# Performance work log

Measured on AMD Instinct MI355X. Metric: run time of the kernel, lower is better.

## Reference

```python
import jax, jax.numpy as jnp
import numpy as np

B, L, H, V = 2, 1024, 64, 32000
HID = 4 * H  # hidden_dim = num_harmonics * 4


def setup_inputs() -> dict:
    key = jax.random.key(0)
    ks = jax.random.split(key, 12)
    freqs = jax.random.normal(ks[0], (B, L, H), dtype=jnp.float32)
    amps = jax.random.uniform(ks[1], (B, L, H), dtype=jnp.float32)  # positive so log1p(sum) is finite
    phases = jax.random.normal(ks[2], (B, L, H), dtype=jnp.float32)
    wave_repr = jnp.concatenate([freqs, amps, phases], axis=-1)  # [B, L, 3H]
    s = 0.05
    return {
        "wave_repr": wave_repr,
        "vocab_frequencies": jax.random.normal(ks[3], (V, H), dtype=jnp.float32),
        "vocab_phases": jax.random.normal(ks[4], (V, H), dtype=jnp.float32) * 0.5,
        "W0": jax.random.normal(ks[5], (3 * H, HID), dtype=jnp.float32) * s,
        "b0": jnp.zeros((HID,), dtype=jnp.float32),
        "W1": jax.random.normal(ks[6], (HID, HID), dtype=jnp.float32) * s,
        "b1": jnp.zeros((HID,), dtype=jnp.float32),
        "W2": jax.random.normal(ks[7], (HID, HID), dtype=jnp.float32) * s,
        "b2": jnp.zeros((HID,), dtype=jnp.float32),
        "Wv": jax.random.normal(ks[8], (HID, V), dtype=jnp.float32) * s,
        "bv": jnp.zeros((V,), dtype=jnp.float32),
        "residual_weights": jnp.full((3,), 0.5, dtype=jnp.float32),
    }


def _gelu(x):
    return jax.nn.gelu(x, approximate=False)  # torch F.gelu default = exact erf


def reference(wave_repr, vocab_frequencies, vocab_phases, W0, b0, W1, b1, W2, b2, Wv, bv, residual_weights):
    h = vocab_frequencies.shape[1]
    freqs = wave_repr[..., :h]
    amps = wave_repr[..., h:2 * h]
    phases = wave_repr[..., 2 * h:]

    # synthesis MLP: layer 0 has no residual; layers 1..2 add weighted residual
    x = _gelu(wave_repr @ W0 + b0)
    for i, (W, b) in enumerate(((W1, b1), (W2, b2)), start=1):
        res = x
        x = _gelu(x @ W + b) + residual_weights[i] * res

    # freq_similarity = -cdist(freqs, vocab_frequencies): expanded as one GEMM
    f2 = jnp.sum(freqs * freqs, axis=-1, keepdims=True)           # [B,L,1]
    v2 = jnp.sum(vocab_frequencies * vocab_frequencies, axis=-1)  # [V]
    cross = jnp.einsum('blh,vh->blv', freqs, vocab_frequencies)   # [B,L,V]
    freq_similarity = -jnp.sqrt(jnp.maximum(f2 + v2 - 2.0 * cross, 0.0))

    # mean_h cos(phase - vocab_phase) via cos(a-b) = cos a cos b + sin a sin b (two GEMMs)
    phase_coherence = (
        jnp.einsum('blh,vh->blv', jnp.cos(phases), jnp.cos(vocab_phases))
        + jnp.einsum('blh,vh->blv', jnp.sin(phases), jnp.sin(vocab_phases))
    ) / h

    amp_energy = jnp.sum(amps, axis=-1, keepdims=True)  # [B,L,1]
    pattern_match = (freq_similarity + 0.5 * phase_coherence) * jnp.log1p(amp_energy)

    synthesis_proj = x @ Wv + bv  # [B,L,V]
    return pattern_match + 0.1 * synthesis_proj
```

## Files before the change

kernel.cpp:

```cpp
#include <hip/hip_runtime.h>
#include <hip/hip_bf16.h>

typedef unsigned short u16;
typedef __attribute__((ext_vector_type(8))) unsigned short u16x8;
typedef __attribute__((ext_vector_type(8))) short short8;
typedef __attribute__((ext_vector_type(4))) float f32x4;

#define VCOLS 32000
#define ASTRIDE 448
#define BSTRIDE 448

__device__ __forceinline__ u16 f2bf(float f) {
    union { float f; unsigned u; } x; x.f = f;
    unsigned r = x.u + 0x7FFF + ((x.u >> 16) & 1);
    return (u16)(r >> 16);
}

__device__ __forceinline__ float gelu_exact(float v) {
    return 0.5f * v * (1.0f + erff(v * 0.70710678118654752f));
}

__device__ __forceinline__ void gload_lds16(const void* g, void* l) {
    __builtin_amdgcn_global_load_lds(
        (const __attribute__((address_space(1))) unsigned int*)g,
        (__attribute__((address_space(3))) unsigned int*)l, 16, 0, 0);
}

#define RP_ROWS 8
__global__ __launch_bounds__(256) void row_prep(
    const float* __restrict__ wr,
    const float* __restrict__ W0, const float* __restrict__ b0,
    const float* __restrict__ W1, const float* __restrict__ b1,
    const float* __restrict__ W2, const float* __restrict__ b2,
    const float* __restrict__ rw,
    u16* __restrict__ Ag, float* __restrict__ rowstats)
{
    __shared__ float in_s[RP_ROWS * 192];
    __shared__ float x_s[RP_ROWS * 256];
    __shared__ float y_s[RP_ROWS * 256];
    __shared__ u16  row_s[RP_ROWS][448];
    __shared__ float la_s[RP_ROWS];

    const int t = threadIdx.x;
    const int r0 = blockIdx.x * RP_ROWS;

    for (int i = t; i < RP_ROWS * 192; i += 256)
        in_s[i] = wr[(size_t)r0 * 192 + i];
    __syncthreads();

    {
        int row = t >> 5, j = t & 31;
        float a0 = in_s[row*192 + j],      a1 = in_s[row*192 + 32 + j];
        float f2p = a0*a0 + a1*a1;
        float ampp = in_s[row*192 + 64 + j] + in_s[row*192 + 96 + j];
        #pragma unroll
        for (int m = 16; m >= 1; m >>= 1) {
            f2p  += __shfl_xor(f2p, m);
            ampp += __shfl_xor(ampp, m);
        }
        if (j == 0) {
            float la = log1pf(ampp);
            la_s[row] = la;
            rowstats[(size_t)(r0+row)*2]     = f2p;
            rowstats[(size_t)(r0+row)*2 + 1] = la;
        }
    }
    const float rw1 = rw[1], rw2 = rw[2];

    float acc[RP_ROWS], res[RP_ROWS];

    #pragma unroll
    for (int r = 0; r < RP_ROWS; ++r) acc[r] = 0.f;
    for (int k0 = 0; k0 < 192; k0 += 16) {
        float w[16];
        #pragma unroll
        for (int e = 0; e < 16; ++e) w[e] = W0[(k0+e)*256 + t];
        #pragma unroll
        for (int e = 0; e < 16; ++e) {
            #pragma unroll
            for (int r = 0; r < RP_ROWS; ++r) acc[r] += in_s[r*192 + k0 + e] * w[e];
        }
    }
    {
        float bb = b0[t];
        #pragma unroll
        for (int r = 0; r < RP_ROWS; ++r) {
            float v = gelu_exact(acc[r] + bb);
            res[r] = v; x_s[r*256 + t] = v;
        }
    }
    __syncthreads();

    #pragma unroll
    for (int r = 0; r < RP_ROWS; ++r) acc[r] = 0.f;
    for (int k0 = 0; k0 < 256; k0 += 16) {
        float w[16];
        #pragma unroll
        for (int e = 0; e < 16; ++e) w[e] = W1[(k0+e)*256 + t];
        #pragma unroll
        for (int e = 0; e < 16; ++e) {
            #pragma unroll
            for (int r = 0; r < RP_ROWS; ++r) acc[r] += x_s[r*256 + k0 + e] * w[e];
        }
    }
    {
        float bb = b1[t];
        #pragma unroll
        for (int r = 0; r < RP_ROWS; ++r) {
            float v = gelu_exact(acc[r] + bb) + rw1 * res[r];
            res[r] = v; y_s[r*256 + t] = v;
        }
    }
    __syncthreads();

    #pragma unroll
    for (int r = 0; r < RP_ROWS; ++r) acc[r] = 0.f;
    for (int k0 = 0; k0 < 256; k0 += 16) {
        float w[16];
        #pragma unroll
        for (int e = 0; e < 16; ++e) w[e] = W2[(k0+e)*256 + t];
        #pragma unroll
        for (int e = 0; e < 16; ++e) {
            #pragma unroll
            for (int r = 0; r < RP_ROWS; ++r) acc[r] += y_s[r*256 + k0 + e] * w[e];
        }
    }
    {
        float bb = b2[t];
        #pragma unroll
        for (int r = 0; r < RP_ROWS; ++r)
            res[r] = gelu_exact(acc[r] + bb) + rw2 * res[r];
    }

    #pragma unroll
    for (int r = 0; r < RP_ROWS; ++r)
        row_s[r][192 + t] = f2bf(0.1f * res[r]);
    if (t < 64) {
        #pragma unroll
        for (int r = 0; r < RP_ROWS; ++r)
            row_s[r][t] = f2bf(in_s[r*192 + t]);
    } else if (t < 128) {
        int h = t - 64;
        #pragma unroll
        for (int r = 0; r < RP_ROWS; ++r) {
            float s, c; __sincosf(in_s[r*192 + 128 + h], &s, &c);
            row_s[r][t] = f2bf(c * (0.5f/64.f) * la_s[r]);
        }
    } else if (t < 192) {
        int h = t - 128;
        #pragma unroll
        for (int r = 0; r < RP_ROWS; ++r) {
            float s, c; __sincosf(in_s[r*192 + 128 + h], &s, &c);
            row_s[r][t] = f2bf(s * (0.5f/64.f) * la_s[r]);
        }
    }
    __syncthreads();

    for (int idx = t; idx < RP_ROWS * 56; idx += 256) {
        int r = idx / 56, c = idx % 56;
        int kt = c >> 3, ac = c & 7;
        int m = r0 + r;
        u16x8 val = *(const u16x8*)&row_s[r][c*8];
        *(u16x8*)(Ag + (size_t)m*ASTRIDE + kt*64 + ((ac ^ (m & 7)) * 8)) = val;
    }
}

__global__ __launch_bounds__(256) void vocab_prep(
    const float* __restrict__ vf, const float* __restrict__ vp,
    const float* __restrict__ Wv,
    u16* __restrict__ Bg, float* __restrict__ v2)
{
    const int t = threadIdx.x;
    const int v0 = blockIdx.x * 64;

    {
        int v = v0 + (t >> 2);
        int q = t & 3;
        int s = v & 7;
        u16x8* baseB = (u16x8*)(Bg + (size_t)v * BSTRIDE);

        const float4* src = (const float4*)(vf + (size_t)v*64 + q*16);
        float ss = 0.f;
        u16 tf[16];
        #pragma unroll
        for (int i = 0; i < 4; ++i) {
            float4 x = src[i];
            ss += x.x*x.x + x.y*x.y + x.z*x.z + x.w*x.w;
            tf[i*4+0] = f2bf(x.x); tf[i*4+1] = f2bf(x.y);
            tf[i*4+2] = f2bf(x.z); tf[i*4+3] = f2bf(x.w);
        }
        u16x8 o0, o1;
        #pragma unroll
        for (int e = 0; e < 8; ++e) { o0[e] = tf[e]; o1[e] = tf[8+e]; }
        baseB[(2*q) ^ s]     = o0;
        baseB[(2*q+1) ^ s]   = o1;

        ss += __shfl_xor(ss, 1);
        ss += __shfl_xor(ss, 2);
        if (q == 0) v2[v] = ss;

        const float4* sp = (const float4*)(vp + (size_t)v*64 + q*16);
        u16 tc[16], ts_[16];
        #pragma unroll
        for (int i = 0; i < 4; ++i) {
            float4 x = sp[i];
            float sn, cs;
            __sincosf(x.x, &sn, &cs); tc[i*4+0] = f2bf(cs); ts_[i*4+0] = f2bf(sn);
            __sincosf(x.y, &sn, &cs); tc[i*4+1] = f2bf(cs); ts_[i*4+1] = f2bf(sn);
            __sincosf(x.z, &sn, &cs); tc[i*4+2] = f2bf(cs); ts_[i*4+2] = f2bf(sn);
            __sincosf(x.w, &sn, &cs); tc[i*4+3] = f2bf(cs); ts_[i*4+3] = f2bf(sn);
        }
        u16x8 c0, c1, s0, s1;
        #pragma unroll
        for (int e = 0; e < 8; ++e) { c0[e]=tc[e]; c1[e]=tc[8+e]; s0[e]=ts_[e]; s1[e]=ts_[8+e]; }
        baseB[8  + ((2*q) ^ s)]   = c0;
        baseB[8  + ((2*q+1) ^ s)] = c1;
        baseB[16 + ((2*q) ^ s)]   = s0;
        baseB[16 + ((2*q+1) ^ s)] = s1;
    }

    {
        int v  = v0 + (t & 63);
        int s  = v & 7;
        int kt = 3 + (t >> 6);
        int kb = (t >> 6) * 64;
        u16x8* baseB = (u16x8*)(Bg + (size_t)v * BSTRIDE);
        #pragma unroll
        for (int i = 0; i < 8; ++i) {
            u16 tmp[8];
            #pragma unroll
            for (int e = 0; e < 8; ++e)
                tmp[e] = f2bf(Wv[(size_t)(kb + i*8 + e) * VCOLS + v]);
            u16x8 o;
            #pragma unroll
            for (int e = 0; e < 8; ++e) o[e] = tmp[e];
            baseB[kt*8 + (i ^ s)] = o;
        }
    }
}

__global__ __launch_bounds__(256) void spectral_main(
    const u16* __restrict__ Ag, const u16* __restrict__ Bg,
    const float* __restrict__ rowstats, const float* __restrict__ v2,
    const float* __restrict__ bv, float* __restrict__ out)
{
    __shared__ u16 As[128 * 64];
    __shared__ u16 Bs[128 * 64];

    const int bid = blockIdx.x;
    const int l   = (bid & 7) * 500 + (bid >> 3);
    const int tm  = l / 250;
    const int tn  = l % 250;
    const int rowA0 = tm * 128;
    const int colB0 = tn * 128;

    const int tid  = threadIdx.x;
    const int wv   = tid >> 6, lane = tid & 63;
    const int wm   = (wv >> 1) * 64, wn = (wv & 1) * 64;
    const int cg   = lane >> 4, ln = lane & 15;

    f32x4 acc[4][4] = {};

    auto stage = [&](int kt) {
        const u16* ab = Ag + (size_t)(rowA0 + wv*32 + (lane >> 3)) * ASTRIDE + kt*64 + (lane & 7)*8;
        u16* al = As + wv*2048 + lane*8;
        #pragma unroll
        for (int c = 0; c < 4; ++c)
            gload_lds16(ab + (size_t)c*8*ASTRIDE, al + c*512);
        const u16* bb = Bg + (size_t)(colB0 + wv*32 + (lane >> 3)) * BSTRIDE + kt*64 + (lane & 7)*8;
        u16* bl = Bs + wv*2048 + lane*8;
        #pragma unroll
        for (int c = 0; c < 4; ++c)
            gload_lds16(bb + (size_t)c*8*BSTRIDE, bl + c*512);
    };

    auto compute = [&]() {
        #pragma unroll
        for (int kk = 0; kk < 2; ++kk) {
            short8 a[4], b[4];
            #pragma unroll
            for (int fr = 0; fr < 4; ++fr) {
                int r = wm + fr*16 + ln;
                a[fr] = *(const short8*)&As[r*64 + (((kk*4 + cg) ^ (ln & 7)) * 8)];
            }
            #pragma unroll
            for (int fc = 0; fc < 4; ++fc) {
                int r = wn + fc*16 + ln;
                b[fc] = *(const short8*)&Bs[r*64 + (((kk*4 + cg) ^ (ln & 7)) * 8)];
            }
            #pragma unroll
            for (int fr = 0; fr < 4; ++fr)
                #pragma unroll
                for (int fc = 0; fc < 4; ++fc)
                    acc[fr][fc] = __builtin_amdgcn_mfma_f32_16x16x32_bf16(
                        a[fr], b[fc], acc[fr][fc], 0, 0, 0);
        }
    };

    stage(0);
    __syncthreads();
    compute();

    {
        float f2m[4][4], lam[4][4], v2n[4], bvn[4];
        #pragma unroll
        for (int fr = 0; fr < 4; ++fr)
            #pragma unroll
            for (int j = 0; j < 4; ++j) {
                int m = rowA0 + wm + fr*16 + cg*4 + j;
                f2m[fr][j] = rowstats[(size_t)2*m];
                lam[fr][j] = rowstats[(size_t)2*m + 1];
            }
        #pragma unroll
        for (int fc = 0; fc < 4; ++fc) {
            int n = colB0 + wn + fc*16 + ln;
            v2n[fc] = v2[n];
            bvn[fc] = bv[n];
        }
        #pragma unroll
        for (int fr = 0; fr < 4; ++fr)
            #pragma unroll
            for (int fc = 0; fc < 4; ++fc)
                #pragma unroll
                for (int j = 0; j < 4; ++j) {
                    float cross = acc[fr][fc][j];
                    float arg = fmaxf(f2m[fr][j] + v2n[fc] - 2.0f*cross, 0.0f);
                    acc[fr][fc][j] = 0.1f*bvn[fc] - lam[fr][j]*sqrtf(arg);
                }
    }

    for (int kt = 1; kt < 7; ++kt) {
        __syncthreads();
        stage(kt);
        __syncthreads();
        compute();
    }

    #pragma unroll
    for (int fr = 0; fr < 4; ++fr)
        #pragma unroll
        for (int fc = 0; fc < 4; ++fc)
            #pragma unroll
            for (int j = 0; j < 4; ++j) {
                int m = rowA0 + wm + fr*16 + cg*4 + j;
                int n = colB0 + wn + fc*16 + ln;
                out[(size_t)m * VCOLS + n] = acc[fr][fc][j];
            }
}

extern "C" void kernel_launch(void* const* d_in, const int* in_sizes, int n_in,
                              void* d_out, int out_size, void* d_ws, size_t ws_size,
                              hipStream_t stream) {
    const float* wave_repr = (const float*)d_in[0];
    const float* vf  = (const float*)d_in[1];
    const float* vp  = (const float*)d_in[2];
    const float* W0  = (const float*)d_in[3];
    const float* b0  = (const float*)d_in[4];
    const float* W1  = (const float*)d_in[5];
    const float* b1  = (const float*)d_in[6];
    const float* W2  = (const float*)d_in[7];
    const float* b2  = (const float*)d_in[8];
    const float* Wv  = (const float*)d_in[9];
    const float* bv  = (const float*)d_in[10];
    const float* rw  = (const float*)d_in[11];
    float* out = (float*)d_out;

    u16*   Ag       = (u16*)d_ws;
    u16*   Bg       = (u16*)((char*)d_ws + 1835008);
    float* rowstats = (float*)((char*)d_ws + 30507008);
    float* v2       = (float*)((char*)d_ws + 30523392);

    hipLaunchKernelGGL(row_prep, dim3(2048 / RP_ROWS), dim3(256), 0, stream,
                       wave_repr, W0, b0, W1, b1, W2, b2, rw, Ag, rowstats);
    hipLaunchKernelGGL(vocab_prep, dim3(VCOLS / 64), dim3(256), 0, stream,
                       vf, vp, Wv, Bg, v2);
    hipLaunchKernelGGL(spectral_main, dim3(16 * 250), dim3(256), 0, stream,
                       Ag, Bg, rowstats, v2, bv, out);
}
```

Before: 470.3 us.

## Double-buffer LDS tiles in main GEMM and stage Wv transpose via shared memory

The main GEMM kernel now keeps two LDS buffers for its A and B tiles. It issues the global-to-LDS load for the next K tile before computing the current one, using explicit vmcnt waits and barriers, so memory latency overlaps with MFMA work. Launch bounds now request two blocks per CU. Separately, the vocab prep kernel reads Wv with coalesced float4 loads into a padded shared tile and transposes from there, replacing strided per-element global reads. The extra LDS per block could limit occupancy, and the hand-written waitcnt logic depends on how many loads are still outstanding.

Result: faster. 458.6 us (-2.5%).

```diff
diff --git a/kernel.cpp b/kernel.cpp
--- a/kernel.cpp
+++ b/kernel.cpp
@@ -170,6 +170,8 @@
     const float* __restrict__ Wv,
     u16* __restrict__ Bg, float* __restrict__ v2)
 {
+    __shared__ float wv_s[64][68];
+
     const int t = threadIdx.x;
     const int v0 = blockIdx.x * 64;
 
@@ -219,33 +221,38 @@
         baseB[16 + ((2*q+1) ^ s)] = s1;
     }
 
-    {
-        int v  = v0 + (t & 63);
-        int s  = v & 7;
-        int kt = 3 + (t >> 6);
-        int kb = (t >> 6) * 64;
-        u16x8* baseB = (u16x8*)(Bg + (size_t)v * BSTRIDE);
-        #pragma unroll
-        for (int i = 0; i < 8; ++i) {
-            u16 tmp[8];
-            #pragma unroll
-            for (int e = 0; e < 8; ++e)
-                tmp[e] = f2bf(Wv[(size_t)(kb + i*8 + e) * VCOLS + v]);
-            u16x8 o;
-            #pragma unroll
-            for (int e = 0; e < 8; ++e) o[e] = tmp[e];
-            baseB[kt*8 + (i ^ s)] = o;
-        }
-    }
-}
-
-__global__ __launch_bounds__(256) void spectral_main(
+    for (int kc = 0; kc < 4; ++kc) {
+        __syncthreads();
+        {
+            int r = t >> 2, q = t & 3;
+            const float4* src = (const float4*)(Wv + (size_t)(kc*64 + r)*VCOLS + v0 + q*16);
+            float4* dst = (float4*)&wv_s[r][q*16];
+            dst[0] = src[0]; dst[1] = src[1]; dst[2] = src[2]; dst[3] = src[3];
+        }
+        __syncthreads();
+        {
+            int v = t & 63, g = t >> 6;
+            int s = (v0 + v) & 7;
+            u16x8* baseB = (u16x8*)(Bg + (size_t)(v0 + v) * BSTRIDE);
+            #pragma unroll
+            for (int cc = 0; cc < 2; ++cc) {
+                int ch = g*2 + cc;
+                u16x8 o;
+                #pragma unroll
+                for (int e = 0; e < 8; ++e) o[e] = f2bf(wv_s[ch*8 + e][v]);
+                baseB[(3 + kc)*8 + (ch ^ s)] = o;
+            }
+        }
+    }
+}
+
+__global__ __launch_bounds__(256, 2) void spectral_main(
     const u16* __restrict__ Ag, const u16* __restrict__ Bg,
     const float* __restrict__ rowstats, const float* __restrict__ v2,
     const float* __restrict__ bv, float* __restrict__ out)
 {
-    __shared__ u16 As[128 * 64];
-    __shared__ u16 Bs[128 * 64];
+    __shared__ u16 As[2][128 * 64];
+    __shared__ u16 Bs[2][128 * 64];
 
     const int bid = blockIdx.x;
     const int l   = (bid & 7) * 500 + (bid >> 3);
@@ -261,32 +268,32 @@
 
     f32x4 acc[4][4] = {};
 
-    auto stage = [&](int kt) {
+    auto stage = [&](int kt, int buf) {
         const u16* ab = Ag + (size_t)(rowA0 + wv*32 + (lane >> 3)) * ASTRIDE + kt*64 + (lane & 7)*8;
-        u16* al = As + wv*2048 + lane*8;
+        u16* al = As[buf] + wv*2048 + lane*8;
         #pragma unroll
         for (int c = 0; c < 4; ++c)
             gload_lds16(ab + (size_t)c*8*ASTRIDE, al + c*512);
         const u16* bb = Bg + (size_t)(colB0 + wv*32 + (lane >> 3)) * BSTRIDE + kt*64 + (lane & 7)*8;
-        u16* bl = Bs + wv*2048 + lane*8;
+        u16* bl = Bs[buf] + wv*2048 + lane*8;
         #pragma unroll
         for (int c = 0; c < 4; ++c)
             gload_lds16(bb + (size_t)c*8*BSTRIDE, bl + c*512);
     };
 
-    auto compute = [&]() {
+    auto compute = [&](int buf) {
         #pragma unroll
         for (int kk = 0; kk < 2; ++kk) {
             short8 a[4], b[4];
             #pragma unroll
             for (int fr = 0; fr < 4; ++fr) {
                 int r = wm + fr*16 + ln;
-                a[fr] = *(const short8*)&As[r*64 + (((kk*4 + cg) ^ (ln & 7)) * 8)];
+                a[fr] = *(const short8*)&As[buf][r*64 + (((kk*4 + cg) ^ (ln & 7)) * 8)];
             }
             #pragma unroll
             for (int fc = 0; fc < 4; ++fc) {
                 int r = wn + fc*16 + ln;
-                b[fc] = *(const short8*)&Bs[r*64 + (((kk*4 + cg) ^ (ln & 7)) * 8)];
+                b[fc] = *(const short8*)&Bs[buf][r*64 + (((kk*4 + cg) ^ (ln & 7)) * 8)];
             }
             #pragma unroll
             for (int fr = 0; fr < 4; ++fr)
@@ -297,43 +304,49 @@
         }
     };
 
-    stage(0);
-    __syncthreads();
-    compute();
-
-    {
-        float f2m[4][4], lam[4][4], v2n[4], bvn[4];
-        #pragma unroll
-        for (int fr = 0; fr < 4; ++fr)
-            #pragma unroll
-            for (int j = 0; j < 4; ++j) {
-                int m = rowA0 + wm + fr*16 + cg*4 + j;
-                f2m[fr][j] = rowstats[(size_t)2*m];
-                lam[fr][j] = rowstats[(size_t)2*m + 1];
-            }
-        #pragma unroll
-        for (int fc = 0; fc < 4; ++fc) {
-            int n = colB0 + wn + fc*16 + ln;
-            v2n[fc] = v2[n];
-            bvn[fc] = bv[n];
-        }
-        #pragma unroll
-        for (int fr = 0; fr < 4; ++fr)
-            #pragma unroll
-            for (int fc = 0; fc < 4; ++fc)
+    stage(0, 0);
+    int cur = 0;
+    for (int kt = 0; kt < 7; ++kt) {
+        if (kt < 6) {
+            stage(kt + 1, cur ^ 1);
+            asm volatile("s_waitcnt vmcnt(8)" ::: "memory");
+        } else {
+            asm volatile("s_waitcnt vmcnt(0)" ::: "memory");
+        }
+        __builtin_amdgcn_s_barrier();
+        compute(cur);
+
+        if (kt == 0) {
+            float f2m[4][4], lam[4][4], v2n[4], bvn[4];
+            #pragma unroll
+            for (int fr = 0; fr < 4; ++fr)
                 #pragma unroll
                 for (int j = 0; j < 4; ++j) {
-                    float cross = acc[fr][fc][j];
-                    float arg = fmaxf(f2m[fr][j] + v2n[fc] - 2.0f*cross, 0.0f);
-                    acc[fr][fc][j] = 0.1f*bvn[fc] - lam[fr][j]*sqrtf(arg);
+                    int m = rowA0 + wm + fr*16 + cg*4 + j;
+                    f2m[fr][j] = rowstats[(size_t)2*m];
+                    lam[fr][j] = rowstats[(size_t)2*m + 1];
                 }
-    }
-
-    for (int kt = 1; kt < 7; ++kt) {
-        __syncthreads();
-        stage(kt);
-        __syncthreads();
-        compute();
+            #pragma unroll
+            for (int fc = 0; fc < 4; ++fc) {
+                int n = colB0 + wn + fc*16 + ln;
+                v2n[fc] = v2[n];
+                bvn[fc] = bv[n];
+            }
+            #pragma unroll
+            for (int fr = 0; fr < 4; ++fr)
+                #pragma unroll
+                for (int fc = 0; fc < 4; ++fc)
+                    #pragma unroll
+                    for (int j = 0; j < 4; ++j) {
+                        float cross = acc[fr][fc][j];
+                        float arg = fmaxf(f2m[fr][j] + v2n[fc] - 2.0f*cross, 0.0f);
+                        acc[fr][fc][j] = 0.1f*bvn[fc] - lam[fr][j]*sqrtf(arg);
+                    }
+        }
+
+        asm volatile("" ::: "memory");
+        __builtin_amdgcn_s_barrier();
+        cur ^= 1;
     }
 
     #pragma unroll
```
